# Optimization experiments

Measured on AMD Instinct MI355X. Metric: run time of the kernel, lower is better.

## Reference

```python
import jax, jax.numpy as jnp
import numpy as np

N_NODES = 4096
HIDDEN = 64
N_REL = 8
N_LAYERS = 2


def setup_inputs() -> dict:
    key = jax.random.key(0)
    k0, k1, k2, k3, k4 = jax.random.split(key, 5)
    node_embed = jax.random.normal(k0, (N_NODES + 1, HIDDEN), dtype=jnp.float32)
    w_self = jax.random.normal(k1, (N_LAYERS, HIDDEN, HIDDEN), dtype=jnp.float32) * 0.02
    w_rel = jax.random.normal(k2, (N_LAYERS, N_REL, HIDDEN, HIDDEN), dtype=jnp.float32) * 0.02
    # dense per-relation adjacency buffer [R, N, N]
    rel_adj = jax.random.uniform(k3, (N_REL, N_NODES, N_NODES), dtype=jnp.float32)
    keyword_ids = jax.random.randint(k4, (64, 32), 0, N_NODES + 1)  # pad id == N_NODES
    return {"node_embed": node_embed, "w_self": w_self, "w_rel": w_rel,
            "rel_adj": rel_adj, "keyword_ids": keyword_ids}


def reference(node_embed, w_self, w_rel, rel_adj, keyword_ids):
    num_nodes = rel_adj.shape[1]
    h = node_embed[:num_nodes]  # [N, D]
    for l in range(w_self.shape[0]):
        out = h @ w_self[l]                                   # self loop [N, D]
        msg = jnp.einsum('rnm,md->rnd', rel_adj, h)           # per-relation aggregation
        out = out + jnp.einsum('rnd,rde->ne', msg, w_rel[l])  # per-relation projection, summed over r
        h = jax.nn.relu(out)
    pad = jnp.zeros((1, h.shape[1]), dtype=h.dtype)
    full_plus_pad = jnp.concatenate([h, pad], axis=0)  # [N+1, D]
    return full_plus_pad[keyword_ids]                  # [B, K, D]
```

## Files before the change

### kernel.cpp

```cpp
#include <hip/hip_runtime.h>

#define N_NODES 4096
#define HID 64
#define NH (N_NODES * HID)

typedef float f32x4 __attribute__((ext_vector_type(4)));
typedef short s16x8 __attribute__((ext_vector_type(8)));

__device__ __forceinline__ short f2bf(float f) {
    union { float f; unsigned u; } v; v.f = f;
    unsigned r = v.u + 0x7fffu + ((v.u >> 16) & 1u);
    return (short)(r >> 16);
}

__global__ __launch_bounds__(256) void proj_kernel(
    const float* __restrict__ h, const float* __restrict__ w_self_l,
    const float* __restrict__ w_rel_l, float* __restrict__ S,
    short* __restrict__ BT)
{
    __shared__ float hs[64][65];
    __shared__ float wt[64][64];
    const int tid = threadIdx.x;
    const int mb = blockIdx.x;
    const int p = blockIdx.y;
    const float* w = (p < 8) ? (w_rel_l + p * 64 * 64) : w_self_l;

    #pragma unroll
    for (int i = 0; i < 4; ++i) {
        int idx4 = tid + 256 * i;
        int row = idx4 >> 4, c = idx4 & 15;
        float4 v = *((const float4*)(h + (size_t)(mb * 64 + row) * HID) + c);
        hs[row][c * 4 + 0] = v.x; hs[row][c * 4 + 1] = v.y;
        hs[row][c * 4 + 2] = v.z; hs[row][c * 4 + 3] = v.w;
    }
    #pragma unroll
    for (int i = 0; i < 4; ++i) {
        int idx4 = tid + 256 * i;
        ((float4*)wt)[idx4] = ((const float4*)w)[idx4];
    }
    __syncthreads();

    const int m = tid & 63;
    const int eb = (tid >> 6) * 16;
    float acc[16];
    #pragma unroll
    for (int j = 0; j < 16; ++j) acc[j] = 0.f;

    #pragma unroll 4
    for (int d = 0; d < 64; ++d) {
        float hv = hs[m][d];
        const float4* wr = (const float4*)&wt[d][eb];
        float4 w0 = wr[0], w1 = wr[1], w2 = wr[2], w3 = wr[3];
        acc[0]  += hv * w0.x; acc[1]  += hv * w0.y; acc[2]  += hv * w0.z; acc[3]  += hv * w0.w;
        acc[4]  += hv * w1.x; acc[5]  += hv * w1.y; acc[6]  += hv * w1.z; acc[7]  += hv * w1.w;
        acc[8]  += hv * w2.x; acc[9]  += hv * w2.y; acc[10] += hv * w2.z; acc[11] += hv * w2.w;
        acc[12] += hv * w3.x; acc[13] += hv * w3.y; acc[14] += hv * w3.z; acc[15] += hv * w3.w;
    }

    if (p < 8) {
        #pragma unroll
        for (int j = 0; j < 16; ++j)
            BT[(size_t)(p * 64 + eb + j) * N_NODES + mb * 64 + m] = f2bf(acc[j]);
    } else {
        #pragma unroll
        for (int j = 0; j < 16; ++j)
            S[(size_t)(mb * 64 + m) * HID + eb + j] = acc[j];
    }
}

__global__ __launch_bounds__(256, 4) void gemm_kernel(
    const float* __restrict__ A, const short* __restrict__ BT,
    float* __restrict__ msg)
{
    __shared__ float As[64][68];
    __shared__ short Bs[64][72];

    const int tid = threadIdx.x;
    const int gid = blockIdx.x;
    const int r  = gid & 7;
    const int rb = (gid >> 3) & 63;
    const int ks = gid >> 9;
    const int wave = tid >> 6, lane = tid & 63;
    const int quad = lane >> 4, l16 = lane & 15;

    const int rA = tid >> 4, cA = tid & 15;
    const int rB = tid >> 3, cB = tid & 7;
    const float* Ag = A  + ((size_t)r * N_NODES + rb * 64) * N_NODES + ks * 2048;
    const short* Bg = BT + ((size_t)r * 64) * N_NODES + ks * 2048;

    f32x4 acc[4];
    #pragma unroll
    for (int nb = 0; nb < 4; ++nb) acc[nb] = (f32x4){0.f, 0.f, 0.f, 0.f};

    f32x4 a_reg[4];
    s16x8 b_reg[2];
    #pragma unroll
    for (int j = 0; j < 4; ++j)
        a_reg[j] = __builtin_nontemporal_load(
            (const f32x4*)(Ag + (size_t)(rA + 16 * j) * N_NODES + cA * 4));
    #pragma unroll
    for (int j = 0; j < 2; ++j)
        b_reg[j] = *(const s16x8*)(Bg + (size_t)(rB + 32 * j) * N_NODES + cB * 8);

    for (int kk = 0; kk < 32; ++kk) {
        __syncthreads();
        #pragma unroll
        for (int j = 0; j < 4; ++j)
            *(f32x4*)&As[rA + 16 * j][cA * 4] = a_reg[j];
        #pragma unroll
        for (int j = 0; j < 2; ++j)
            *(s16x8*)&Bs[rB + 32 * j][cB * 8] = b_reg[j];

        if (kk < 31) {
            const int k0 = (kk + 1) * 64;
            #pragma unroll
            for (int j = 0; j < 4; ++j)
                a_reg[j] = __builtin_nontemporal_load(
                    (const f32x4*)(Ag + (size_t)(rA + 16 * j) * N_NODES + k0 + cA * 4));
            #pragma unroll
            for (int j = 0; j < 2; ++j)
                b_reg[j] = *(const s16x8*)(Bg + (size_t)(rB + 32 * j) * N_NODES + k0 + cB * 8);
        }
        __syncthreads();

        #pragma unroll
        for (int s = 0; s < 2; ++s) {
            f32x4 af0 = *(const f32x4*)&As[wave * 16 + l16][s * 32 + quad * 8];
            f32x4 af1 = *(const f32x4*)&As[wave * 16 + l16][s * 32 + quad * 8 + 4];
            s16x8 af;
            af[0] = f2bf(af0[0]); af[1] = f2bf(af0[1]); af[2] = f2bf(af0[2]); af[3] = f2bf(af0[3]);
            af[4] = f2bf(af1[0]); af[5] = f2bf(af1[1]); af[6] = f2bf(af1[2]); af[7] = f2bf(af1[3]);
            #pragma unroll
            for (int nb = 0; nb < 4; ++nb) {
                s16x8 bfr = *(const s16x8*)&Bs[l16 + nb * 16][s * 32 + quad * 8];
                acc[nb] = __builtin_amdgcn_mfma_f32_16x16x32_bf16(af, bfr, acc[nb], 0, 0, 0);
            }
        }
    }

    float* mo = msg + ((size_t)(r * 2 + ks)) * NH;
    #pragma unroll
    for (int nb = 0; nb < 4; ++nb) {
        #pragma unroll
        for (int i = 0; i < 4; ++i) {
            int orow = rb * 64 + wave * 16 + quad * 4 + i;
            mo[(size_t)orow * HID + nb * 16 + l16] = acc[nb][i];
        }
    }
}

__global__ __launch_bounds__(256) void relu_kernel(
    const float* __restrict__ S, const float* __restrict__ msg, float* __restrict__ hout)
{
    int i = blockIdx.x * 256 + threadIdx.x;
    float4 s = ((const float4*)S)[i];
    #pragma unroll
    for (int p = 0; p < 16; ++p) {
        float4 m = ((const float4*)(msg + (size_t)p * NH))[i];
        s.x += m.x; s.y += m.y; s.z += m.z; s.w += m.w;
    }
    float4 o;
    o.x = fmaxf(s.x, 0.f); o.y = fmaxf(s.y, 0.f);
    o.z = fmaxf(s.z, 0.f); o.w = fmaxf(s.w, 0.f);
    ((float4*)hout)[i] = o;
}

__global__ __launch_bounds__(256) void gather_kernel(
    const float* __restrict__ h2, const int* __restrict__ kw, float* __restrict__ out)
{
    int e = blockIdx.x * 256 + threadIdx.x;
    int ki = e >> 6, d = e & 63;
    int id = kw[ki];
    out[e] = ((unsigned)id < (unsigned)N_NODES) ? h2[(size_t)id * HID + d] : 0.f;
}

extern "C" void kernel_launch(void* const* d_in, const int* in_sizes, int n_in,
                              void* d_out, int out_size, void* d_ws, size_t ws_size,
                              hipStream_t stream) {
    const float* node_embed = (const float*)d_in[0];
    const float* w_self     = (const float*)d_in[1];
    const float* w_rel      = (const float*)d_in[2];
    const float* rel_adj    = (const float*)d_in[3];
    const int*   kw         = (const int*)d_in[4];
    float* out = (float*)d_out;

    float* msg = (float*)d_ws;
    float* S   = msg + 16 * NH;
    float* h1  = S + NH;
    float* h2  = h1 + NH;
    short* BT  = (short*)(h2 + NH);

    const float* hin = node_embed;
    float* houts[2] = {h1, h2};
    for (int l = 0; l < 2; ++l) {
        proj_kernel<<<dim3(64, 9), 256, 0, stream>>>(
            hin, w_self + (size_t)l * 64 * 64, w_rel + (size_t)l * 8 * 64 * 64, S, BT);
        gemm_kernel<<<1024, 256, 0, stream>>>(rel_adj, BT, msg);
        relu_kernel<<<256, 256, 0, stream>>>(S, msg, houts[l]);
        hin = houts[l];
    }
    gather_kernel<<<512, 256, 0, stream>>>(h2, kw, out);
}
```

Baseline: 825.5 us.

## Double-buffer GEMM LDS tiles and convert A to bf16 before LDS store

The adjacency GEMM now keeps two LDS buffers of bf16 tiles, so each iteration needs one barrier instead of two. The fp32 A tile is converted to bf16 once when written to LDS, rather than stored as fp32 and converted per wave at fragment load, which also halves A's LDS footprint. Global loads are issued two tiles ahead to overlap with the MFMA work. The cost is more register pressure from the prefetch, plus hand-placed waitcnt and sched barriers that must be correct for synchronisation.

```diff
diff --git a/kernel.cpp b/kernel.cpp
--- a/kernel.cpp
+++ b/kernel.cpp
@@ -5,6 +5,7 @@
 #define NH (N_NODES * HID)
 
 typedef float f32x4 __attribute__((ext_vector_type(4)));
+typedef short s16x4 __attribute__((ext_vector_type(4)));
 typedef short s16x8 __attribute__((ext_vector_type(8)));
 
 __device__ __forceinline__ short f2bf(float f) {
@@ -72,8 +73,8 @@
     const float* __restrict__ A, const short* __restrict__ BT,
     float* __restrict__ msg)
 {
-    __shared__ float As[64][68];
-    __shared__ short Bs[64][72];
+    __shared__ __attribute__((aligned(16))) short As[2][64 * 72];
+    __shared__ __attribute__((aligned(16))) short Bs[2][64 * 72];
 
     const int tid = threadIdx.x;
     const int gid = blockIdx.x;
@@ -92,49 +93,55 @@
     #pragma unroll
     for (int nb = 0; nb < 4; ++nb) acc[nb] = (f32x4){0.f, 0.f, 0.f, 0.f};
 
-    f32x4 a_reg[4];
-    s16x8 b_reg[2];
-    #pragma unroll
-    for (int j = 0; j < 4; ++j)
-        a_reg[j] = __builtin_nontemporal_load(
-            (const f32x4*)(Ag + (size_t)(rA + 16 * j) * N_NODES + cA * 4));
-    #pragma unroll
-    for (int j = 0; j < 2; ++j)
-        b_reg[j] = *(const s16x8*)(Bg + (size_t)(rB + 32 * j) * N_NODES + cB * 8);
-
-    for (int kk = 0; kk < 32; ++kk) {
-        __syncthreads();
+    f32x4 a_nx[4];
+    s16x8 b_nx[2];
+    auto load_tile = [&](int t) {
+        const int k0 = t * 64;
         #pragma unroll
         for (int j = 0; j < 4; ++j)
-            *(f32x4*)&As[rA + 16 * j][cA * 4] = a_reg[j];
+            a_nx[j] = __builtin_nontemporal_load(
+                (const f32x4*)(Ag + (size_t)(rA + 16 * j) * N_NODES + k0 + cA * 4));
         #pragma unroll
         for (int j = 0; j < 2; ++j)
-            *(s16x8*)&Bs[rB + 32 * j][cB * 8] = b_reg[j];
-
-        if (kk < 31) {
-            const int k0 = (kk + 1) * 64;
-            #pragma unroll
-            for (int j = 0; j < 4; ++j)
-                a_reg[j] = __builtin_nontemporal_load(
-                    (const f32x4*)(Ag + (size_t)(rA + 16 * j) * N_NODES + k0 + cA * 4));
-            #pragma unroll
-            for (int j = 0; j < 2; ++j)
-                b_reg[j] = *(const s16x8*)(Bg + (size_t)(rB + 32 * j) * N_NODES + k0 + cB * 8);
-        }
-        __syncthreads();
-
+            b_nx[j] = *(const s16x8*)(Bg + (size_t)(rB + 32 * j) * N_NODES + k0 + cB * 8);
+    };
+    auto write_tile = [&](int b) {
+        #pragma unroll
+        for (int j = 0; j < 4; ++j) {
+            s16x4 av;
+            av[0] = f2bf(a_nx[j][0]); av[1] = f2bf(a_nx[j][1]);
+            av[2] = f2bf(a_nx[j][2]); av[3] = f2bf(a_nx[j][3]);
+            *(s16x4*)&As[b][(rA + 16 * j) * 72 + cA * 4] = av;
+        }
+        #pragma unroll
+        for (int j = 0; j < 2; ++j)
+            *(s16x8*)&Bs[b][(rB + 32 * j) * 72 + cB * 8] = b_nx[j];
+    };
+
+    load_tile(0);
+    write_tile(0);
+    load_tile(1);
+    asm volatile("s_waitcnt lgkmcnt(0)" ::: "memory");
+    __builtin_amdgcn_s_barrier();
+
+    #pragma unroll 2
+    for (int t = 0; t < 32; ++t) {
+        const int b = t & 1;
         #pragma unroll
         for (int s = 0; s < 2; ++s) {
-            f32x4 af0 = *(const f32x4*)&As[wave * 16 + l16][s * 32 + quad * 8];
-            f32x4 af1 = *(const f32x4*)&As[wave * 16 + l16][s * 32 + quad * 8 + 4];
-            s16x8 af;
-            af[0] = f2bf(af0[0]); af[1] = f2bf(af0[1]); af[2] = f2bf(af0[2]); af[3] = f2bf(af0[3]);
-            af[4] = f2bf(af1[0]); af[5] = f2bf(af1[1]); af[6] = f2bf(af1[2]); af[7] = f2bf(af1[3]);
+            s16x8 af = *(const s16x8*)&As[b][(wave * 16 + l16) * 72 + s * 32 + quad * 8];
             #pragma unroll
             for (int nb = 0; nb < 4; ++nb) {
-                s16x8 bfr = *(const s16x8*)&Bs[l16 + nb * 16][s * 32 + quad * 8];
+                s16x8 bfr = *(const s16x8*)&Bs[b][(nb * 16 + l16) * 72 + s * 32 + quad * 8];
                 acc[nb] = __builtin_amdgcn_mfma_f32_16x16x32_bf16(af, bfr, acc[nb], 0, 0, 0);
             }
+        }
+        if (t < 31) {
+            __builtin_amdgcn_sched_barrier(0);
+            write_tile(b ^ 1);
+            if (t < 30) load_tile(t + 2);
+            asm volatile("s_waitcnt lgkmcnt(0)" ::: "memory");
+            __builtin_amdgcn_s_barrier();
         }
     }
 
```

New measurement: 821.0 us. About the same (-0.5%).
